# Optimization experiments

Hardware: AMD Instinct MI355X
Metric: run time of the kernel (lower is better)

## Reference

```python
import jax, jax.numpy as jnp
import numpy as np

B, L = 2048, 64          # batch, seq_len (title length)
H, DK = 20, 20           # heads, per-head dim (d_k = d_v = 20)
V, D = 50000, 300        # vocab, word embedding dim
HD = H * DK              # 400


def setup_inputs() -> dict:
    key = jax.random.key(0)
    ks = jax.random.split(key, 12)
    n = lambda k, shape, sc: jax.random.normal(k, shape, dtype=jnp.float32) * sc
    return {
        "text": jax.random.randint(ks[0], (B, L), 0, V),
        "emb": n(ks[1], (V, D), 0.1),
        "WQ": n(ks[2], (D, HD), 0.05), "bQ": jnp.zeros((HD,), jnp.float32),
        "WK": n(ks[3], (D, HD), 0.05), "bK": jnp.zeros((HD,), jnp.float32),
        "WV": n(ks[4], (D, HD), 0.05), "bV": jnp.zeros((HD,), jnp.float32),
        "W1": n(ks[5], (HD, 200), 0.05), "b1": jnp.zeros((200,), jnp.float32),
        "W2": n(ks[6], (200, 1), 0.05), "b2": jnp.zeros((1,), jnp.float32),
    }


def reference(text, emb, WQ, bQ, WK, bK, WV, bV, W1, b1, W2, b2):
    # Embedding lookup (dropout is identity at eval)
    x = emb[text]                                            # [B, L, D]
    b, l = x.shape[0], x.shape[1]

    # Multi-head self-attention with unstable exp-softmax (faithful to source)
    q = (x @ WQ + bQ).reshape(b, l, H, DK)                   # [B, L, H, DK]
    k = (x @ WK + bK).reshape(b, l, H, DK)
    v = (x @ WV + bV).reshape(b, l, H, DK)
    scores = jnp.einsum("bqhd,bkhd->bhqk", q, k) / np.float32(np.sqrt(DK))
    scores = jnp.exp(scores)                                 # [B, H, L, L]
    attn = scores / (jnp.sum(scores, axis=-1, keepdims=True) + 1e-8)
    ctx = jnp.einsum("bhqk,bkhd->bqhd", attn, v).reshape(b, l, HD)  # [B, L, 400]

    # Additive attention pooling (linear -> tanh -> linear -> exp-normalize -> weighted sum)
    e = jnp.tanh(ctx @ W1 + b1)                              # [B, L, 200]
    alpha = jnp.exp(e @ W2 + b2)                             # [B, L, 1]
    alpha = alpha / (jnp.sum(alpha, axis=1, keepdims=True) + 1e-8)
    return jnp.sum(ctx * alpha, axis=1)                      # [B, 400]
```

## Files before the change

kernel.cpp:

```cpp
#include <hip/hip_runtime.h>
#include <hip/hip_bf16.h>

#define B_   2048
#define L_   64
#define H_   20
#define DK_  20
#define D_   300
#define HD_  400
#define F1_  200

typedef __attribute__((ext_vector_type(8))) short short8;
typedef __attribute__((ext_vector_type(4))) float f32x4;

#define WQKV_TILES   800
#define W1_TILES     169
#define W1_OFF_U16   409600
#define WS_NEEDED    992256

__device__ __forceinline__ float b2f(unsigned short u) {
    union { unsigned int i; float f; } v; v.i = ((unsigned int)u) << 16; return v.f;
}
__device__ __forceinline__ unsigned short f2b(float f) {
    union { float f; unsigned int i; } v; v.f = f;
    unsigned int x = v.i;
    return (unsigned short)((x + 0x7fffu + ((x >> 16) & 1u)) >> 16);
}
__device__ __forceinline__ float rlane(float v, int l) {
    return __int_as_float(__builtin_amdgcn_readlane(__float_as_int(v), l));
}

__global__ void pack_weights(const float* __restrict__ WQ, const float* __restrict__ WK,
                             const float* __restrict__ WV, const float* __restrict__ W1,
                             unsigned short* __restrict__ wsp)
{
    const int tid  = blockIdx.x * 256 + threadIdx.x;
    const int frag = tid >> 6, l = tid & 63;
    if (frag >= WQKV_TILES + W1_TILES) return;
    const int octet = l >> 4, lo = l & 15;
    unsigned short v[8];
    if (frag < WQKV_TILES) {
        const int hg = frag / 160, r = frag % 160, kt = r / 16, nt = r % 16;
        const int nl = nt * 16 + lo;
        const int sel = (nl < 240) ? nl / 80 : 0;
        const int within = nl % 80;
        const int h2 = within / 20, d = within % 20;
        const int col = (hg * 4 + h2) * 20 + d;
        const float* W = (sel == 0) ? WQ : (sel == 1) ? WK : WV;
        #pragma unroll
        for (int j = 0; j < 8; ++j) {
            const int k = kt * 32 + octet * 8 + j;
            const float f = (nl < 240 && k < 300) ? W[k * 400 + col] : 0.f;
            v[j] = f2b(f);
        }
    } else {
        const int f2 = frag - WQKV_TILES, kt = f2 / 13, nt = f2 % 13;
        const int n = nt * 16 + lo;
        #pragma unroll
        for (int j = 0; j < 8; ++j) {
            const int k = kt * 32 + octet * 8 + j;
            const float f = (n < 200 && k < 400) ? W1[k * 200 + n] : 0.f;
            v[j] = f2b(f);
        }
    }
    unsigned short* dst = wsp + (long)frag * 512 + l * 8;
    *(ushort4*)(dst)     = make_ushort4(v[0], v[1], v[2], v[3]);
    *(ushort4*)(dst + 4) = make_ushort4(v[4], v[5], v[6], v[7]);
}

__global__ __launch_bounds__(1024, 4)
void te_mfma(const int* __restrict__ text,
             const float* __restrict__ emb,
             const float* __restrict__ bQ, const float* __restrict__ bK,
             const float* __restrict__ bV, const float* __restrict__ b1,
             const float* __restrict__ W2, const float* __restrict__ b2,
             const unsigned short* __restrict__ wsp,
             float* __restrict__ out)
{
    __shared__ unsigned short x_pack[4 * 10 * 64 * 8];
    __shared__ unsigned short ctxA[4 * 13 * 64 * 8];
    __shared__ unsigned short trans[16384];
    __shared__ unsigned short vB[8192];
    __shared__ float rsum_s[4 * 64];
    __shared__ float bqkv_s[3 * 400];
    __shared__ float b1_s[208];
    __shared__ float w2_s[208];
    __shared__ int   text_s[64];
    __shared__ float aacc_s[64], alpha_s[64];
    __shared__ float inv_asum_s;

    const int b = blockIdx.x;
    const int t = threadIdx.x;
    const int l = t & 63;
    const int w = t >> 6;

    {
        unsigned int* xz = (unsigned int*)x_pack;
        for (int i = t; i < 10240; i += 1024) xz[i] = 0u;
        unsigned int* cz = (unsigned int*)ctxA;
        for (int i = t; i < 13312; i += 1024) cz[i] = 0u;
        unsigned int* tz = (unsigned int*)trans;
        for (int i = t; i < 8192; i += 1024) tz[i] = 0u;
        unsigned int* vz = (unsigned int*)vB;
        for (int i = t; i < 4096; i += 1024) {
            const int lane_v = (i >> 2) & 63;
            const int dnt    = (i >> 8) & 1;
            vz[i] = (dnt == 1 && (lane_v & 15) == 4) ? 0x3F803F80u : 0u;
        }
        for (int i = t; i < 1200; i += 1024)
            bqkv_s[i] = (i < 400) ? bQ[i] : (i < 800) ? bK[i - 400] : bV[i - 800];
        if (t < 208) { b1_s[t] = (t < 200) ? b1[t] : 0.f; w2_s[t] = (t < 200) ? W2[t] : 0.f; }
        if (t >= 208 && t < 272) aacc_s[t - 208] = 0.f;
        if (t >= 272 && t < 336) text_s[t - 272] = text[b * L_ + (t - 272)];
    }
    __syncthreads();

    for (int u = t; u < 64 * 75; u += 1024) {
        const int r = u / 75, c4 = u - r * 75, k = c4 * 4;
        const float4 f = *(const float4*)(emb + (long)text_s[r] * D_ + k);
        const int mt = r >> 4, kt = k >> 5;
        const int ld = (r & 15) + ((k & 31) >> 3) * 16;
        const int off = ((mt * 10 + kt) * 64 + ld) * 8 + (k & 7);
        ushort4 o; o.x = f2b(f.x); o.y = f2b(f.y); o.z = f2b(f.z); o.w = f2b(f.w);
        *(ushort4*)(x_pack + off) = o;
    }
    __syncthreads();

    for (int hg = 0; hg < 5; ++hg) {
        if (w < 15) {
            f32x4 accA[4];
            #pragma unroll
            for (int mt = 0; mt < 4; ++mt) accA[mt] = (f32x4){0.f, 0.f, 0.f, 0.f};
            for (int kt = 0; kt < 10; ++kt) {
                short8 a[4];
                #pragma unroll
                for (int mt = 0; mt < 4; ++mt)
                    a[mt] = *(const short8*)(x_pack + ((mt * 10 + kt) * 64 + l) * 8);
                const short8 bf = *(const short8*)(wsp + ((long)(hg * 160 + kt * 16 + w) * 512) + l * 8);
                #pragma unroll
                for (int mt = 0; mt < 4; ++mt)
                    accA[mt] = __builtin_amdgcn_mfma_f32_16x16x32_bf16(a[mt], bf, accA[mt], 0, 0, 0);
            }
            const int nl = w * 16 + (l & 15);
            const int sel = nl / 80, within = nl % 80;
            const int h2 = within / 20, d = within % 20;
            const float bias = bqkv_s[sel * 400 + (hg * 4 + h2) * 20 + d];
            #pragma unroll
            for (int mt = 0; mt < 4; ++mt)
                #pragma unroll
                for (int ii = 0; ii < 4; ++ii) {
                    const int tok = mt * 16 + (l >> 4) * 4 + ii;
                    const unsigned short us = f2b(accA[mt][ii] + bias);
                    if (sel == 0) {
                        const int ld = (tok & 15) + (d >> 3) * 16;
                        trans[((h2 * 4 + mt) * 64 + ld) * 8 + (d & 7)] = us;
                    } else if (sel == 1) {
                        const int ld = (tok & 15) + (d >> 3) * 16;
                        trans[8192 + ((h2 * 4 + mt) * 64 + ld) * 8 + (d & 7)] = us;
                    } else {
                        const int ktv = tok >> 5;
                        const int ld  = (d & 15) + ((tok & 31) >> 3) * 16;
                        vB[(((h2 * 2 + ktv) * 2 + (d >> 4)) * 64 + ld) * 8 + (tok & 7)] = us;
                    }
                }
        }
        __syncthreads();

        const int h  = w >> 2;
        {
            const int jt = w & 3;
            f32x4 accS[4];
            #pragma unroll
            for (int mt = 0; mt < 4; ++mt) accS[mt] = (f32x4){0.f, 0.f, 0.f, 0.f};
            short8 qa[4];
            #pragma unroll
            for (int mt = 0; mt < 4; ++mt)
                qa[mt] = *(const short8*)(trans + ((h * 4 + mt) * 64 + l) * 8);
            const short8 kb = *(const short8*)(trans + 8192 + ((h * 4 + jt) * 64 + l) * 8);
            #pragma unroll
            for (int mt = 0; mt < 4; ++mt)
                accS[mt] = __builtin_amdgcn_mfma_f32_16x16x32_bf16(qa[mt], kb, accS[mt], 0, 0, 0);
            __syncthreads();
            const int jtok = jt * 16 + (l & 15);
            const int ktp = jtok >> 5;
            #pragma unroll
            for (int mt = 0; mt < 4; ++mt)
                #pragma unroll
                for (int ii = 0; ii < 4; ++ii) {
                    const int itok = mt * 16 + (l >> 4) * 4 + ii;
                    const float pv = __expf(accS[mt][ii] * 0.22360679774997896f);
                    const int ld = (itok & 15) + ((jtok & 31) >> 3) * 16;
                    trans[(((h * 4 + mt) * 2 + ktp) * 64 + ld) * 8 + (jtok & 7)] = f2b(pv);
                }
        }
        __syncthreads();

        {
            const int dnt = (w >> 1) & 1;
            const int mh  = w & 1;
            f32x4 accC[2];
            accC[0] = (f32x4){0.f, 0.f, 0.f, 0.f};
            accC[1] = (f32x4){0.f, 0.f, 0.f, 0.f};
            #pragma unroll
            for (int ktc = 0; ktc < 2; ++ktc) {
                const short8 vb = *(const short8*)(vB + (((h * 2 + ktc) * 2 + dnt) * 64 + l) * 8);
                #pragma unroll
                for (int mi = 0; mi < 2; ++mi) {
                    const int mt = mh * 2 + mi;
                    const short8 pa = *(const short8*)(trans + (((h * 4 + mt) * 2 + ktc) * 64 + l) * 8);
                    accC[mi] = __builtin_amdgcn_mfma_f32_16x16x32_bf16(pa, vb, accC[mi], 0, 0, 0);
                }
            }
            if (dnt == 1 && (l & 15) == 4) {
                #pragma unroll
                for (int mi = 0; mi < 2; ++mi)
                    #pragma unroll
                    for (int ii = 0; ii < 4; ++ii)
                        rsum_s[h * 64 + (mh * 2 + mi) * 16 + (l >> 4) * 4 + ii] = accC[mi][ii];
            }
            __syncthreads();
            if (hg < 4) {
                unsigned int* tz = (unsigned int*)trans;
                for (int i = t; i < 8192; i += 1024) tz[i] = 0u;
            }
            const int dloc = dnt * 16 + (l & 15);
            if (dloc < 20) {
                const int col = (hg * 4 + h) * 20 + dloc;
                const int ktx = col >> 5;
                const int ldx = ((col & 31) >> 3) * 16;
                #pragma unroll
                for (int mi = 0; mi < 2; ++mi) {
                    const int mt = mh * 2 + mi;
                    #pragma unroll
                    for (int ii = 0; ii < 4; ++ii) {
                        const int tok = mt * 16 + (l >> 4) * 4 + ii;
                        const float inv = 1.f / (rsum_s[h * 64 + tok] + 1e-8f);
                        ctxA[((mt * 13 + ktx) * 64 + (tok & 15) + ldx) * 8 + (col & 7)] =
                            f2b(accC[mi][ii] * inv);
                    }
                }
            }
        }
        __syncthreads();
    }

    if (w < 13) {
        f32x4 accD[4];
        #pragma unroll
        for (int mt = 0; mt < 4; ++mt) accD[mt] = (f32x4){0.f, 0.f, 0.f, 0.f};
        for (int kt = 0; kt < 13; ++kt) {
            short8 ca[4];
            #pragma unroll
            for (int mt = 0; mt < 4; ++mt)
                ca[mt] = *(const short8*)(ctxA + ((mt * 13 + kt) * 64 + l) * 8);
            const short8 wb = *(const short8*)(wsp + W1_OFF_U16 + ((long)(kt * 13 + w) * 512) + l * 8);
            #pragma unroll
            for (int mt = 0; mt < 4; ++mt)
                accD[mt] = __builtin_amdgcn_mfma_f32_16x16x32_bf16(ca[mt], wb, accD[mt], 0, 0, 0);
        }
        const int colb = w * 16 + (l & 15);
        const float b1v = b1_s[colb], w2v = w2_s[colb];
        #pragma unroll
        for (int mt = 0; mt < 4; ++mt)
            #pragma unroll
            for (int ii = 0; ii < 4; ++ii) {
                const float x = accD[mt][ii] + b1v;
                const float ex = __expf(2.f * x);
                float v = ((ex - 1.f) / (ex + 1.f)) * w2v;
                v += __shfl_xor(v, 1, 64); v += __shfl_xor(v, 2, 64);
                v += __shfl_xor(v, 4, 64); v += __shfl_xor(v, 8, 64);
                if ((l & 15) == 0)
                    atomicAdd(&aacc_s[mt * 16 + (l >> 4) * 4 + ii], v);
            }
    }
    __syncthreads();

    if (t < 64) {
        const float a = __expf(aacc_s[t] + b2[0]);
        alpha_s[t] = a;
        float s = a;
        s += __shfl_xor(s, 32, 64); s += __shfl_xor(s, 16, 64);
        s += __shfl_xor(s, 8, 64);  s += __shfl_xor(s, 4, 64);
        s += __shfl_xor(s, 2, 64);  s += __shfl_xor(s, 1, 64);
        if (t == 0) inv_asum_s = 1.f / (s + 1e-8f);
    }
    __syncthreads();

    if (t < HD_) {
        const int c = t;
        const int ktx = c >> 5, ldo = ((c & 31) >> 3) * 16, el = c & 7;
        float a = 0.f;
        for (int tok = 0; tok < 64; ++tok) {
            const unsigned short us =
                ctxA[(((tok >> 4) * 13 + ktx) * 64 + (tok & 15) + ldo) * 8 + el];
            a = fmaf(b2f(us), alpha_s[tok], a);
        }
        out[(long)b * HD_ + c] = a * inv_asum_s;
    }
}

#define XS   324
#define CS   404
#define QS   21
#define SS   66

__global__ __launch_bounds__(512, 2)
void te_fused_fb(const int* __restrict__ text, const float* __restrict__ emb,
                 const float* __restrict__ WQ, const float* __restrict__ bQ,
                 const float* __restrict__ WK, const float* __restrict__ bK,
                 const float* __restrict__ WV, const float* __restrict__ bV,
                 const float* __restrict__ W1, const float* __restrict__ b1,
                 const float* __restrict__ W2, const float* __restrict__ b2,
                 float* __restrict__ out)
{
    __shared__ int            text_s[L_];
    __shared__ unsigned short x_s[L_ * XS];
    __shared__ unsigned short ctx_s[L_ * CS];
    __shared__ float          qkv_s[3 * 2 * L_ * QS];
    __shared__ unsigned short sc_s[2 * L_ * SS];
    __shared__ float          aacc_s[L_], alpha_s[L_];
    __shared__ float          inv_asum_s;

    const int b = blockIdx.x, t = threadIdx.x, lane = t & 63, wv = t >> 6;
    if (t < 64) text_s[t] = text[b * L_ + t];
    if (t >= 64 && t < 128) aacc_s[t - 64] = 0.f;
    __syncthreads();
    for (int u = t; u < L_ * 75; u += 512) {
        int l = u / 75, c4 = u - l * 75;
        const float4 f = *(const float4*)(emb + (long)text_s[l] * D_ + c4 * 4);
        ushort4 o; o.x = f2b(f.x); o.y = f2b(f.y); o.z = f2b(f.z); o.w = f2b(f.w);
        *(ushort4*)(x_s + l * XS + c4 * 4) = o;
    }
    __syncthreads();
    for (int hp = 0; hp < H_ / 2; ++hp) {
        const int h0 = hp * 2;
        if (t < 480) {
            const int rt = t & 15, ct = t >> 4, r0 = rt * 4, qc = ct * 4;
            const int sel = qc / 40, rem = qc - sel * 40, hh = rem / 20, cc = rem - hh * 20;
            const float* W = (sel == 0) ? WQ : (sel == 1) ? WK : WV;
            const float* bias = (sel == 0) ? bQ : (sel == 1) ? bK : bV;
            const int col0 = (h0 + hh) * 20 + cc;
            float acc[4][4];
            #pragma unroll
            for (int j = 0; j < 4; ++j) {
                const float bj = bias[col0 + j];
                acc[0][j] = bj; acc[1][j] = bj; acc[2][j] = bj; acc[3][j] = bj;
            }
            const float* Wp = W + col0;
            for (int c4 = 0; c4 < 75; ++c4) {
                const int d0 = c4 * 4;
                float xv[4][4]; float4 wvv[4];
                #pragma unroll
                for (int i = 0; i < 4; ++i) {
                    ushort4 xu = *(const ushort4*)(x_s + (r0 + i) * XS + d0);
                    xv[i][0] = b2f(xu.x); xv[i][1] = b2f(xu.y);
                    xv[i][2] = b2f(xu.z); xv[i][3] = b2f(xu.w);
                }
                #pragma unroll
                for (int dd = 0; dd < 4; ++dd)
                    wvv[dd] = *(const float4*)(Wp + (long)(d0 + dd) * HD_);
                #pragma unroll
                for (int dd = 0; dd < 4; ++dd)
                    #pragma unroll
                    for (int i = 0; i < 4; ++i) {
                        acc[i][0] = fmaf(xv[i][dd], wvv[dd].x, acc[i][0]);
                        acc[i][1] = fmaf(xv[i][dd], wvv[dd].y, acc[i][1]);
                        acc[i][2] = fmaf(xv[i][dd], wvv[dd].z, acc[i][2]);
                        acc[i][3] = fmaf(xv[i][dd], wvv[dd].w, acc[i][3]);
                    }
            }
            #pragma unroll
            for (int i = 0; i < 4; ++i)
                #pragma unroll
                for (int j = 0; j < 4; ++j)
                    qkv_s[((sel * 2 + hh) * L_ + r0 + i) * QS + cc + j] = acc[i][j];
        }
        __syncthreads();
        {
            const int j = lane, ig = wv & 3, hh = wv >> 2;
            float qreg[20], kreg[20];
            const float* qrow = &qkv_s[((0 * 2 + hh) * L_ + j) * QS];
            const float* krow = &qkv_s[((1 * 2 + hh) * L_ + j) * QS];
            #pragma unroll
            for (int d = 0; d < 20; ++d) { qreg[d] = qrow[d]; kreg[d] = krow[d]; }
            for (int ii = 0; ii < 16; ++ii) {
                const int i = ig * 16 + ii;
                float s = 0.f;
                #pragma unroll
                for (int d = 0; d < 20; ++d) s = fmaf(rlane(qreg[d], i), kreg[d], s);
                sc_s[(hh * L_ + i) * SS + j] = f2b(__expf(s * 0.22360679774997896f));
            }
        }
        __syncthreads();
        {
            const int i = lane, dg = wv, head = dg >> 2, dv0 = (dg & 3) * 5;
            float vreg[5];
            #pragma unroll
            for (int m = 0; m < 5; ++m)
                vreg[m] = qkv_s[((2 * 2 + head) * L_ + i) * QS + dv0 + m];
            float acc[5] = {0.f, 0.f, 0.f, 0.f, 0.f};
            float rsum = 0.f;
            const unsigned short* prow = &sc_s[(head * L_ + i) * SS];
            for (int jj = 0; jj < 64; ++jj) {
                const float p = b2f(prow[jj]);
                rsum += p;
                #pragma unroll
                for (int m = 0; m < 5; ++m) acc[m] = fmaf(p, rlane(vreg[m], jj), acc[m]);
            }
            const float inv = 1.f / (rsum + 1e-8f);
            const int col0 = (h0 + head) * 20 + dv0;
            #pragma unroll
            for (int m = 0; m < 5; ++m) ctx_s[i * CS + col0 + m] = f2b(acc[m] * inv);
        }
        __syncthreads();
    }
    for (int tau = t; tau < 800; tau += 512) {
        const int rt = tau & 15, cm = tau >> 4, r0 = rt * 4, m0 = cm * 4;
        float acc[4][4];
        #pragma unroll
        for (int j = 0; j < 4; ++j) {
            const float bj = b1[m0 + j];
            acc[0][j] = bj; acc[1][j] = bj; acc[2][j] = bj; acc[3][j] = bj;
        }
        for (int c4 = 0; c4 < 100; ++c4) {
            const int c0 = c4 * 4;
            float cv[4][4]; float4 wv1[4];
            #pragma unroll
            for (int i = 0; i < 4; ++i) {
                ushort4 cu = *(const ushort4*)(ctx_s + (r0 + i) * CS + c0);
                cv[i][0] = b2f(cu.x); cv[i][1] = b2f(cu.y);
                cv[i][2] = b2f(cu.z); cv[i][3] = b2f(cu.w);
            }
            #pragma unroll
            for (int dd = 0; dd < 4; ++dd)
                wv1[dd] = *(const float4*)(W1 + (long)(c0 + dd) * F1_ + m0);
            #pragma unroll
            for (int dd = 0; dd < 4; ++dd)
                #pragma unroll
                for (int i = 0; i < 4; ++i) {
                    acc[i][0] = fmaf(cv[i][dd], wv1[dd].x, acc[i][0]);
                    acc[i][1] = fmaf(cv[i][dd], wv1[dd].y, acc[i][1]);
                    acc[i][2] = fmaf(cv[i][dd], wv1[dd].z, acc[i][2]);
                    acc[i][3] = fmaf(cv[i][dd], wv1[dd].w, acc[i][3]);
                }
        }
        float w2l[4];
        #pragma unroll
        for (int j = 0; j < 4; ++j) w2l[j] = W2[m0 + j];
        #pragma unroll
        for (int i = 0; i < 4; ++i) {
            float ap = 0.f;
            #pragma unroll
            for (int j = 0; j < 4; ++j) ap += tanhf(acc[i][j]) * w2l[j];
            atomicAdd(&aacc_s[r0 + i], ap);
        }
    }
    __syncthreads();
    if (t < 64) {
        const float a = __expf(aacc_s[t] + b2[0]);
        alpha_s[t] = a;
        float s = a;
        s += __shfl_xor(s, 32, 64); s += __shfl_xor(s, 16, 64);
        s += __shfl_xor(s, 8, 64);  s += __shfl_xor(s, 4, 64);
        s += __shfl_xor(s, 2, 64);  s += __shfl_xor(s, 1, 64);
        if (t == 0) inv_asum_s = 1.f / (s + 1e-8f);
    }
    __syncthreads();
    if (t < HD_) {
        float a = 0.f;
        for (int l2 = 0; l2 < 64; ++l2)
            a = fmaf(b2f(ctx_s[l2 * CS + t]), alpha_s[l2], a);
        out[(long)b * HD_ + t] = a * inv_asum_s;
    }
}

extern "C" void kernel_launch(void* const* d_in, const int* in_sizes, int n_in,
                              void* d_out, int out_size, void* d_ws, size_t ws_size,
                              hipStream_t stream) {
    const int*   text = (const int*)d_in[0];
    const float* emb  = (const float*)d_in[1];
    const float* WQ   = (const float*)d_in[2];
    const float* bQ   = (const float*)d_in[3];
    const float* WK   = (const float*)d_in[4];
    const float* bK   = (const float*)d_in[5];
    const float* WV   = (const float*)d_in[6];
    const float* bV   = (const float*)d_in[7];
    const float* W1   = (const float*)d_in[8];
    const float* b1   = (const float*)d_in[9];
    const float* W2   = (const float*)d_in[10];
    const float* b2   = (const float*)d_in[11];
    float*       out  = (float*)d_out;

    if (ws_size >= (size_t)WS_NEEDED) {
        unsigned short* wsp = (unsigned short*)d_ws;
        const int total_frag_threads = (WQKV_TILES + W1_TILES) * 64;
        pack_weights<<<(total_frag_threads + 255) / 256, 256, 0, stream>>>(WQ, WK, WV, W1, wsp);
        te_mfma<<<B_, 1024, 0, stream>>>(text, emb, bQ, bK, bV, b1, W2, b2, wsp, out);
    } else {
        te_fused_fb<<<B_, 512, 0, stream>>>(text, emb, WQ, bQ, WK, bK, WV, bV,
                                            W1, b1, W2, b2, out);
    }
}
```

Baseline: 422.8 us.

## Split fused kernel into attention and pooling kernels with bf16 ctx workspace

```diff
diff --git a/kernel.cpp b/kernel.cpp
--- a/kernel.cpp
+++ b/kernel.cpp
@@ -16,6 +16,9 @@
 #define W1_TILES     169
 #define W1_OFF_U16   409600
 #define WS_NEEDED    992256
+#define CTX_OFF_B    1048576
+#define CTX_BYTES    (2048L * 64 * 400 * 2)
+#define WS_FULL      (CTX_OFF_B + CTX_BYTES)
 
 __device__ __forceinline__ float b2f(unsigned short u) {
     union { unsigned int i; float f; } v; v.i = ((unsigned int)u) << 16; return v.f;
@@ -29,9 +32,346 @@
     return __int_as_float(__builtin_amdgcn_readlane(__float_as_int(v), l));
 }
 
-__global__ void pack_weights(const float* __restrict__ WQ, const float* __restrict__ WK,
-                             const float* __restrict__ WV, const float* __restrict__ W1,
-                             unsigned short* __restrict__ wsp)
+__global__ void pack_weights_new(const float* __restrict__ WQ, const float* __restrict__ WK,
+                                 const float* __restrict__ WV, const float* __restrict__ W1,
+                                 unsigned short* __restrict__ wsp)
+{
+    const int tid  = blockIdx.x * 256 + threadIdx.x;
+    const int frag = tid >> 6, l = tid & 63;
+    if (frag >= WQKV_TILES + W1_TILES) return;
+    const int octet = l >> 4, lo = l & 15;
+    unsigned short v[8];
+    if (frag < WQKV_TILES) {
+        const int hg = frag / 80, r = frag % 80, kt = r / 8, nt = r % 8;
+        const int nl = nt * 16 + lo;
+        const int sel = (nl < 120) ? nl / 40 : 0;
+        const int within = nl % 40;
+        const int h2 = within / 20, d = within % 20;
+        const int col = (hg * 2 + h2) * 20 + d;
+        const float* W = (sel == 0) ? WQ : (sel == 1) ? WK : WV;
+        #pragma unroll
+        for (int j = 0; j < 8; ++j) {
+            const int k = kt * 32 + octet * 8 + j;
+            const float f = (nl < 120 && k < 300) ? W[k * 400 + col] : 0.f;
+            v[j] = f2b(f);
+        }
+    } else {
+        const int f2 = frag - WQKV_TILES, kt = f2 / 13, nt = f2 % 13;
+        const int n = nt * 16 + lo;
+        #pragma unroll
+        for (int j = 0; j < 8; ++j) {
+            const int k = kt * 32 + octet * 8 + j;
+            const float f = (n < 200 && k < 400) ? W1[k * 200 + n] : 0.f;
+            v[j] = f2b(f);
+        }
+    }
+    unsigned short* dst = wsp + (long)frag * 512 + l * 8;
+    *(ushort4*)(dst)     = make_ushort4(v[0], v[1], v[2], v[3]);
+    *(ushort4*)(dst + 4) = make_ushort4(v[4], v[5], v[6], v[7]);
+}
+
+__global__ __launch_bounds__(512, 4)
+void te_attn(const int* __restrict__ text,
+             const float* __restrict__ emb,
+             const float* __restrict__ bQ, const float* __restrict__ bK,
+             const float* __restrict__ bV,
+             const unsigned short* __restrict__ wsp,
+             unsigned short* __restrict__ ctx_ws)
+{
+    __shared__ unsigned short x_pack[4 * 10 * 64 * 8];
+    __shared__ unsigned short trans[8192];
+    __shared__ unsigned short vB[4096];
+    __shared__ unsigned short ctx_stage[64 * 40];
+    __shared__ float bqkv_s[1200];
+    __shared__ float rsum_s[2 * 64];
+    __shared__ int   text_s[64];
+
+    const int b = blockIdx.x;
+    const int t = threadIdx.x;
+    const int l = t & 63;
+    const int w = t >> 6;
+
+    {
+        unsigned int* xz = (unsigned int*)x_pack;
+        for (int i = t; i < 10240; i += 512) xz[i] = 0u;
+        unsigned int* tz = (unsigned int*)trans;
+        for (int i = t; i < 4096; i += 512) tz[i] = 0u;
+        unsigned int* vz = (unsigned int*)vB;
+        for (int i = t; i < 2048; i += 512) {
+            const int tile = i >> 8;
+            const int lane = (i & 255) >> 2;
+            vz[i] = ((tile & 1) == 1 && (lane & 15) == 4) ? 0x3F803F80u : 0u;
+        }
+        for (int i = t; i < 1200; i += 512)
+            bqkv_s[i] = (i < 400) ? bQ[i] : (i < 800) ? bK[i - 400] : bV[i - 800];
+        if (t < 64) text_s[t] = text[b * L_ + t];
+    }
+    __syncthreads();
+
+    for (int u = t; u < 64 * 75; u += 512) {
+        const int r = u / 75, c4 = u - r * 75, k = c4 * 4;
+        const float4 f = *(const float4*)(emb + (long)text_s[r] * D_ + k);
+        const int mt = r >> 4, kt = k >> 5;
+        const int ld = (r & 15) + ((k & 31) >> 3) * 16;
+        const int off = ((mt * 10 + kt) * 64 + ld) * 8 + (k & 7);
+        ushort4 o; o.x = f2b(f.x); o.y = f2b(f.y); o.z = f2b(f.z); o.w = f2b(f.w);
+        *(ushort4*)(x_pack + off) = o;
+    }
+    __syncthreads();
+
+    for (int hg = 0; hg < 10; ++hg) {
+        if (hg > 0) {
+            for (int u = t; u < 640; u += 512) {
+                const int row = u / 10, c4 = u - row * 10;
+                const ushort4 v = *(const ushort4*)(ctx_stage + row * 40 + c4 * 4);
+                *(ushort4*)(ctx_ws + ((long)(b * 64 + row)) * 400 + (hg - 1) * 40 + c4 * 4) = v;
+            }
+        }
+        {
+            f32x4 accA[4];
+            #pragma unroll
+            for (int mt = 0; mt < 4; ++mt) accA[mt] = (f32x4){0.f, 0.f, 0.f, 0.f};
+            for (int kt = 0; kt < 10; ++kt) {
+                short8 a[4];
+                #pragma unroll
+                for (int mt = 0; mt < 4; ++mt)
+                    a[mt] = *(const short8*)(x_pack + ((mt * 10 + kt) * 64 + l) * 8);
+                const short8 bf = *(const short8*)(wsp + ((long)(hg * 80 + kt * 8 + w) * 512) + l * 8);
+                #pragma unroll
+                for (int mt = 0; mt < 4; ++mt)
+                    accA[mt] = __builtin_amdgcn_mfma_f32_16x16x32_bf16(a[mt], bf, accA[mt], 0, 0, 0);
+            }
+            const int nl = w * 16 + (l & 15);
+            if (nl < 120) {
+                const int sel = nl / 40, within = nl % 40;
+                const int h2 = within / 20, d = within % 20;
+                const float bias = bqkv_s[sel * 400 + (hg * 2 + h2) * 20 + d];
+                #pragma unroll
+                for (int mt = 0; mt < 4; ++mt)
+                    #pragma unroll
+                    for (int ii = 0; ii < 4; ++ii) {
+                        const int tok = mt * 16 + (l >> 4) * 4 + ii;
+                        const unsigned short us = f2b(accA[mt][ii] + bias);
+                        if (sel == 0) {
+                            const int ld = (tok & 15) + (d >> 3) * 16;
+                            trans[((h2 * 4 + mt) * 64 + ld) * 8 + (d & 7)] = us;
+                        } else if (sel == 1) {
+                            const int ld = (tok & 15) + (d >> 3) * 16;
+                            trans[4096 + ((h2 * 4 + (tok >> 4)) * 64 + ld) * 8 + (d & 7)] = us;
+                        } else {
+                            const int ktv = tok >> 5;
+                            const int ld  = (d & 15) + ((tok & 31) >> 3) * 16;
+                            vB[(((h2 * 2 + ktv) * 2 + (d >> 4)) * 64 + ld) * 8 + (tok & 7)] = us;
+                        }
+                    }
+            }
+        }
+        __syncthreads();
+
+        const int h  = w >> 2;
+        {
+            const int jt = w & 3;
+            f32x4 accS[4];
+            #pragma unroll
+            for (int mt = 0; mt < 4; ++mt) accS[mt] = (f32x4){0.f, 0.f, 0.f, 0.f};
+            short8 qa[4];
+            #pragma unroll
+            for (int mt = 0; mt < 4; ++mt)
+                qa[mt] = *(const short8*)(trans + ((h * 4 + mt) * 64 + l) * 8);
+            const short8 kb = *(const short8*)(trans + 4096 + ((h * 4 + jt) * 64 + l) * 8);
+            #pragma unroll
+            for (int mt = 0; mt < 4; ++mt)
+                accS[mt] = __builtin_amdgcn_mfma_f32_16x16x32_bf16(qa[mt], kb, accS[mt], 0, 0, 0);
+            __syncthreads();
+            const int jtok = jt * 16 + (l & 15);
+            const int ktp = jtok >> 5;
+            #pragma unroll
+            for (int mt = 0; mt < 4; ++mt)
+                #pragma unroll
+                for (int ii = 0; ii < 4; ++ii) {
+                    const int itok = mt * 16 + (l >> 4) * 4 + ii;
+                    const float pv = __expf(accS[mt][ii] * 0.22360679774997896f);
+                    const int ld = (itok & 15) + ((jtok & 31) >> 3) * 16;
+                    trans[(((h * 4 + mt) * 2 + ktp) * 64 + ld) * 8 + (jtok & 7)] = f2b(pv);
+                }
+        }
+        __syncthreads();
+
+        {
+            const int dnt = (w >> 1) & 1;
+            const int mh  = w & 1;
+            f32x4 accC[2];
+            accC[0] = (f32x4){0.f, 0.f, 0.f, 0.f};
+            accC[1] = (f32x4){0.f, 0.f, 0.f, 0.f};
+            #pragma unroll
+            for (int ktc = 0; ktc < 2; ++ktc) {
+                const short8 vb = *(const short8*)(vB + (((h * 2 + ktc) * 2 + dnt) * 64 + l) * 8);
+                #pragma unroll
+                for (int mi = 0; mi < 2; ++mi) {
+                    const int mt = mh * 2 + mi;
+                    const short8 pa = *(const short8*)(trans + (((h * 4 + mt) * 2 + ktc) * 64 + l) * 8);
+                    accC[mi] = __builtin_amdgcn_mfma_f32_16x16x32_bf16(pa, vb, accC[mi], 0, 0, 0);
+                }
+            }
+            if (dnt == 1 && (l & 15) == 4) {
+                #pragma unroll
+                for (int mi = 0; mi < 2; ++mi)
+                    #pragma unroll
+                    for (int ii = 0; ii < 4; ++ii)
+                        rsum_s[h * 64 + (mh * 2 + mi) * 16 + (l >> 4) * 4 + ii] = accC[mi][ii];
+            }
+            __syncthreads();
+            if (hg < 9) {
+                unsigned int* tz = (unsigned int*)trans;
+                for (int i = t; i < 4096; i += 512) tz[i] = 0u;
+            }
+            const int dloc = dnt * 16 + (l & 15);
+            if (dloc < 20) {
+                const int cl = h * 20 + dloc;
+                #pragma unroll
+                for (int mi = 0; mi < 2; ++mi) {
+                    const int mt = mh * 2 + mi;
+                    #pragma unroll
+                    for (int ii = 0; ii < 4; ++ii) {
+                        const int tok = mt * 16 + (l >> 4) * 4 + ii;
+                        const float inv = 1.f / (rsum_s[h * 64 + tok] + 1e-8f);
+                        ctx_stage[tok * 40 + cl] = f2b(accC[mi][ii] * inv);
+                    }
+                }
+            }
+        }
+        __syncthreads();
+    }
+
+    for (int u = t; u < 640; u += 512) {
+        const int row = u / 10, c4 = u - row * 10;
+        const ushort4 v = *(const ushort4*)(ctx_stage + row * 40 + c4 * 4);
+        *(ushort4*)(ctx_ws + ((long)(b * 64 + row)) * 400 + 9 * 40 + c4 * 4) = v;
+    }
+}
+
+__global__ __launch_bounds__(512, 4)
+void te_pool(const unsigned short* __restrict__ ctx_ws,
+             const float* __restrict__ b1, const float* __restrict__ W2,
+             const float* __restrict__ b2,
+             const unsigned short* __restrict__ wsp,
+             float* __restrict__ out)
+{
+    __shared__ unsigned short ctxA[4 * 13 * 64 * 8];
+    __shared__ float b1_s[208], w2_s[208];
+    __shared__ float aacc_s[64], alpha_s[64];
+    __shared__ float inv_asum_s;
+
+    const int b = blockIdx.x;
+    const int t = threadIdx.x;
+    const int l = t & 63;
+    const int w = t >> 6;
+
+    {
+        unsigned int* cz = (unsigned int*)ctxA;
+        for (int i = t; i < 1024; i += 512) {
+            const int mt = i >> 8;
+            cz[(mt * 13 + 12) * 256 + (i & 255)] = 0u;
+        }
+        if (t < 208) { b1_s[t] = (t < 200) ? b1[t] : 0.f; w2_s[t] = (t < 200) ? W2[t] : 0.f; }
+        if (t >= 208 && t < 272) aacc_s[t - 208] = 0.f;
+    }
+    __syncthreads();
+
+    for (int u = t; u < 6400; u += 512) {
+        const int row = u / 100, c4 = u - row * 100;
+        const int col = c4 * 4;
+        const ushort4 v = *(const ushort4*)(ctx_ws + ((long)(b * 64 + row)) * 400 + col);
+        const int mt = row >> 4, ktx = col >> 5;
+        const int ld = (row & 15) + ((col & 31) >> 3) * 16;
+        *(ushort4*)(ctxA + ((mt * 13 + ktx) * 64 + ld) * 8 + (col & 7)) = v;
+    }
+    __syncthreads();
+
+    {
+        f32x4 accD[2][4];
+        #pragma unroll
+        for (int g = 0; g < 2; ++g)
+            #pragma unroll
+            for (int mt = 0; mt < 4; ++mt) accD[g][mt] = (f32x4){0.f, 0.f, 0.f, 0.f};
+        const int nta = w, ntb = w + 8;
+        for (int kt = 0; kt < 13; ++kt) {
+            short8 ca[4];
+            #pragma unroll
+            for (int mt = 0; mt < 4; ++mt)
+                ca[mt] = *(const short8*)(ctxA + ((mt * 13 + kt) * 64 + l) * 8);
+            const short8 wb0 = *(const short8*)(wsp + W1_OFF_U16 + ((long)(kt * 13 + nta) * 512) + l * 8);
+            #pragma unroll
+            for (int mt = 0; mt < 4; ++mt)
+                accD[0][mt] = __builtin_amdgcn_mfma_f32_16x16x32_bf16(ca[mt], wb0, accD[0][mt], 0, 0, 0);
+            if (ntb < 13) {
+                const short8 wb1 = *(const short8*)(wsp + W1_OFF_U16 + ((long)(kt * 13 + ntb) * 512) + l * 8);
+                #pragma unroll
+                for (int mt = 0; mt < 4; ++mt)
+                    accD[1][mt] = __builtin_amdgcn_mfma_f32_16x16x32_bf16(ca[mt], wb1, accD[1][mt], 0, 0, 0);
+            }
+        }
+        float part[4][4];
+        #pragma unroll
+        for (int mt = 0; mt < 4; ++mt)
+            #pragma unroll
+            for (int ii = 0; ii < 4; ++ii) part[mt][ii] = 0.f;
+        #pragma unroll
+        for (int g = 0; g < 2; ++g) {
+            const int ntv = (g == 0) ? nta : ntb;
+            if (ntv < 13) {
+                const int colb = ntv * 16 + (l & 15);
+                const float b1v = b1_s[colb], w2v = w2_s[colb];
+                #pragma unroll
+                for (int mt = 0; mt < 4; ++mt)
+                    #pragma unroll
+                    for (int ii = 0; ii < 4; ++ii) {
+                        const float x = accD[g][mt][ii] + b1v;
+                        const float ex = __expf(2.f * x);
+                        part[mt][ii] += ((ex - 1.f) / (ex + 1.f)) * w2v;
+                    }
+            }
+        }
+        #pragma unroll
+        for (int mt = 0; mt < 4; ++mt)
+            #pragma unroll
+            for (int ii = 0; ii < 4; ++ii) {
+                float v = part[mt][ii];
+                v += __shfl_xor(v, 1, 64); v += __shfl_xor(v, 2, 64);
+                v += __shfl_xor(v, 4, 64); v += __shfl_xor(v, 8, 64);
+                if ((l & 15) == 0)
+                    atomicAdd(&aacc_s[mt * 16 + (l >> 4) * 4 + ii], v);
+            }
+    }
+    __syncthreads();
+
+    if (t < 64) {
+        const float a = __expf(aacc_s[t] + b2[0]);
+        alpha_s[t] = a;
+        float s = a;
+        s += __shfl_xor(s, 32, 64); s += __shfl_xor(s, 16, 64);
+        s += __shfl_xor(s, 8, 64);  s += __shfl_xor(s, 4, 64);
+        s += __shfl_xor(s, 2, 64);  s += __shfl_xor(s, 1, 64);
+        if (t == 0) inv_asum_s = 1.f / (s + 1e-8f);
+    }
+    __syncthreads();
+
+    if (t < HD_) {
+        const int c = t;
+        const int ktx = c >> 5, ldo = ((c & 31) >> 3) * 16, el = c & 7;
+        float a = 0.f;
+        for (int tok = 0; tok < 64; ++tok) {
+            const unsigned short us =
+                ctxA[(((tok >> 4) * 13 + ktx) * 64 + (tok & 15) + ldo) * 8 + el];
+            a = fmaf(b2f(us), alpha_s[tok], a);
+        }
+        out[(long)b * HD_ + c] = a * inv_asum_s;
+    }
+}
+
+__global__ void pack_weights_old(const float* __restrict__ WQ, const float* __restrict__ WK,
+                                 const float* __restrict__ WV, const float* __restrict__ W1,
+                                 unsigned short* __restrict__ wsp)
 {
     const int tid  = blockIdx.x * 256 + threadIdx.x;
     const int frag = tid >> 6, l = tid & 63;
@@ -490,10 +830,16 @@
     const float* b2   = (const float*)d_in[11];
     float*       out  = (float*)d_out;
 
-    if (ws_size >= (size_t)WS_NEEDED) {
+    const int total_frag_threads = (WQKV_TILES + W1_TILES) * 64;
+    if (ws_size >= (size_t)WS_FULL) {
+        unsigned short* wsp    = (unsigned short*)d_ws;
+        unsigned short* ctx_ws = (unsigned short*)((char*)d_ws + CTX_OFF_B);
+        pack_weights_new<<<(total_frag_threads + 255) / 256, 256, 0, stream>>>(WQ, WK, WV, W1, wsp);
+        te_attn<<<B_, 512, 0, stream>>>(text, emb, bQ, bK, bV, wsp, ctx_ws);
+        te_pool<<<B_, 512, 0, stream>>>(ctx_ws, b1, W2, b2, wsp, out);
+    } else if (ws_size >= (size_t)WS_NEEDED) {
         unsigned short* wsp = (unsigned short*)d_ws;
-        const int total_frag_threads = (WQKV_TILES + W1_TILES) * 64;
-        pack_weights<<<(total_frag_threads + 255) / 256, 256, 0, stream>>>(WQ, WK, WV, W1, wsp);
+        pack_weights_old<<<(total_frag_threads + 255) / 256, 256, 0, stream>>>(WQ, WK, WV, W1, wsp);
         te_mfma<<<B_, 1024, 0, stream>>>(text, emb, bQ, bK, bV, b1, W2, b2, wsp, out);
     } else {
         te_fused_fb<<<B_, 512, 0, stream>>>(text, emb, WQ, bQ, WK, bK, WV, bV,
```

After: 411.8 us. 2.6% less time.
